# Kernel tuning notes

Hardware: AMD Instinct MI355X
Metric: run time of the kernel (lower is better)

The kernel has to match this reference:

```python
import jax, jax.numpy as jnp
import numpy as np

N_NODES = 40000
N_EDGES = 640000
IN_CH = 128
HID1, HID2 = 512, 256
OUT_CH = 2
NUM_GRAPHS = 16
EPS = 1e-5


def layer_norm(x, g, b):
    mu = jnp.mean(x, axis=-1, keepdims=True)
    var = jnp.mean(jnp.square(x - mu), axis=-1, keepdims=True)
    return (x - mu) * jax.lax.rsqrt(var + EPS) * g + b


def gcn_conv(x, src, dst, ew, W, b, n_nodes):
    # PyG GCNConv: x' = x @ W; symmetric normalization with self-loops already
    # appended to (src, dst, ew) by the caller; bias added after aggregation.
    xw = x @ W                                            # [N, out]
    deg = jax.ops.segment_sum(ew, dst, num_segments=n_nodes)
    dinv = jnp.where(deg > 0, jax.lax.rsqrt(deg), 0.0)    # deg^{-1/2}, 0 for isolated
    norm = dinv[src] * ew * dinv[dst]                     # [E+N]
    msgs = norm[:, None] * xw[src]                        # gather + scale
    out = jax.ops.segment_sum(msgs, dst, num_segments=n_nodes)
    return out + b


def setup_inputs() -> dict:
    key = jax.random.key(0)
    ks = jax.random.split(key, 12)
    x = jax.random.normal(ks[0], (N_NODES, IN_CH), dtype=jnp.float32)
    edge_index = jax.random.randint(ks[1], (2, N_EDGES), 0, N_NODES, dtype=jnp.int64)
    edge_weight = jax.random.uniform(ks[2], (N_EDGES,), dtype=jnp.float32)
    batch = jnp.sort(jax.random.randint(ks[3], (N_NODES,), 0, NUM_GRAPHS, dtype=jnp.int64))
    # parameters (Glorot-ish scale)
    W1 = jax.random.normal(ks[4], (IN_CH, HID1), dtype=jnp.float32) / np.sqrt(IN_CH)
    b1 = jnp.zeros((HID1,), dtype=jnp.float32)
    g1 = jnp.ones((HID1,), dtype=jnp.float32)
    be1 = jnp.zeros((HID1,), dtype=jnp.float32)
    W2 = jax.random.normal(ks[5], (HID1, HID2), dtype=jnp.float32) / np.sqrt(HID1)
    b2 = jnp.zeros((HID2,), dtype=jnp.float32)
    g2 = jnp.ones((HID2,), dtype=jnp.float32)
    be2 = jnp.zeros((HID2,), dtype=jnp.float32)
    Wfc = jax.random.normal(ks[6], (HID2, OUT_CH), dtype=jnp.float32) / np.sqrt(HID2)
    bfc = jnp.zeros((OUT_CH,), dtype=jnp.float32)
    return {"x": x, "edge_index": edge_index, "edge_weight": edge_weight,
            "batch": batch, "W1": W1, "b1": b1, "g1": g1, "be1": be1,
            "W2": W2, "b2": b2, "g2": g2, "be2": be2, "Wfc": Wfc, "bfc": bfc}


def reference(x, edge_index, edge_weight, batch, W1, b1, g1, be1, W2, b2, g2, be2, Wfc, bfc):
    n = x.shape[0]
    loop = jnp.arange(n, dtype=edge_index.dtype)
    src = jnp.concatenate([edge_index[0], loop])
    dst = jnp.concatenate([edge_index[1], loop])
    ew = jnp.concatenate([edge_weight, jnp.ones((n,), dtype=edge_weight.dtype)])

    h = gcn_conv(x, src, dst, ew, W1, b1, n)
    h = layer_norm(jax.nn.relu(h), g1, be1)          # dropout = identity (eval)
    h3 = gcn_conv(h, src, dst, ew, W2, b2, n)
    h3 = layer_norm(jax.nn.relu(h3), g2, be2)

    # global mean pool over graph ids
    sums = jax.ops.segment_sum(h3, batch, num_segments=NUM_GRAPHS)
    cnts = jax.ops.segment_sum(jnp.ones((n,), dtype=h3.dtype), batch, num_segments=NUM_GRAPHS)
    pooled = sums / jnp.maximum(cnts, 1.0)[:, None]
    out = pooled @ Wfc + bfc
    return h3, out
```

## Files before the change

kernel.cpp:

```cpp
#include <hip/hip_runtime.h>
#include <hip/hip_bf16.h>

#define N_NODES   40000
#define N_EDGES   640000
#define IN_CH     128
#define HID1      512
#define HID2      256
#define OUT_CH    2
#define NUM_GRAPHS 16
#define EPSF      1e-5f
#define SCAN_NB   157
#define FIXSC     1048576.0f

typedef unsigned short u16;
typedef unsigned int   u32;
typedef unsigned long long u64;
using short8 = __attribute__((ext_vector_type(8))) short;
using f32x4  = __attribute__((ext_vector_type(4))) float;

__device__ __forceinline__ float b2f(u16 u) {
    return __uint_as_float(((u32)u) << 16);
}
__device__ __forceinline__ u16 f2b(float f) {
    u32 u = __float_as_uint(f);
    u32 r = (u + 0x7FFFu + ((u >> 16) & 1u)) >> 16;
    return (u16)r;
}
__device__ __forceinline__ void gload_lds16(const u16* g, u16* l) {
    __builtin_amdgcn_global_load_lds((const __attribute__((address_space(1))) u32*)g,
                                     (__attribute__((address_space(3))) u32*)l, 16, 0, 0);
}

__global__ __launch_bounds__(256) void pack_kernel(const int* __restrict__ dst,
                                                   const float* __restrict__ ew,
                                                   u64* __restrict__ packed,
                                                   int* __restrict__ eoff) {
    int t = blockIdx.x * blockDim.x + threadIdx.x;
    if (t >= N_EDGES) return;
    int d = dst[t];
    u64 inc = (1ull << 40) | (u64)__float2uint_rn(ew[t] * FIXSC);
    u64 old = atomicAdd(&packed[d], inc);
    eoff[t] = (int)(old >> 40);
}

__global__ __launch_bounds__(256) void scan_p1_kernel(const u64* __restrict__ packed,
                                                      float* __restrict__ dinv,
                                                      int* __restrict__ rowptr,
                                                      int* __restrict__ blocksum) {
    __shared__ int sd[256];
    const int t = threadIdx.x;
    const int i = blockIdx.x * 256 + t;
    int v = 0;
    if (i < N_NODES) {
        u64 p = packed[i];
        v = (int)(p >> 40);
        float deg = (float)(p & ((1ull << 40) - 1)) * (1.0f / FIXSC);
        dinv[i] = rsqrtf(deg + 1.0f);
    }
    sd[t] = v;
    __syncthreads();
    for (int off = 1; off < 256; off <<= 1) {
        int u = (t >= off) ? sd[t - off] : 0;
        __syncthreads();
        sd[t] += u;
        __syncthreads();
    }
    if (i < N_NODES) rowptr[i] = sd[t] - v;
    if (t == 255) blocksum[blockIdx.x] = sd[255];
}

__global__ __launch_bounds__(256) void scan_p2_kernel(int* __restrict__ blocksum,
                                                      int* __restrict__ bprefix,
                                                      const int* __restrict__ batch,
                                                      int* __restrict__ gstart) {
    __shared__ int sd[256];
    const int t = threadIdx.x;
    const int v = (t < SCAN_NB) ? blocksum[t] : 0;
    sd[t] = v;
    __syncthreads();
    for (int off = 1; off < 256; off <<= 1) {
        int u = (t >= off) ? sd[t - off] : 0;
        __syncthreads();
        sd[t] += u;
        __syncthreads();
    }
    bprefix[t] = sd[t] - v;
    if (t <= NUM_GRAPHS) {
        int lo = 0, hi = N_NODES;
        while (lo < hi) {
            int mid = (lo + hi) >> 1;
            if (batch[mid] < t) lo = mid + 1; else hi = mid;
        }
        gstart[t] = lo;
    }
}

__global__ __launch_bounds__(256) void scan_p3_kernel(int* __restrict__ rowptr,
                                                      const int* __restrict__ bprefix) {
    const int i = blockIdx.x * 256 + threadIdx.x;
    if (i < N_NODES) rowptr[i] += bprefix[blockIdx.x];
    if (i == 0) rowptr[N_NODES] = N_EDGES;
}

__global__ __launch_bounds__(256) void scatter_kernel(const int* __restrict__ src,
                                                      const int* __restrict__ dst,
                                                      const float* __restrict__ ew,
                                                      const float* __restrict__ dinv,
                                                      const int* __restrict__ rowptr,
                                                      const int* __restrict__ eoff,
                                                      int2* __restrict__ csr_pair) {
    int t = blockIdx.x * blockDim.x + threadIdx.x;
    if (t >= N_EDGES) return;
    int s = src[t], d = dst[t];
    int pos = rowptr[d] + eoff[t];
    float norm = dinv[s] * ew[t] * dinv[d];
    int2 pr; pr.x = s; pr.y = __float_as_int(norm);
    csr_pair[pos] = pr;
}

__global__ __launch_bounds__(256) void prep_kernel(const float* __restrict__ x,
                                                   u16* __restrict__ xb,
                                                   const float* __restrict__ W1,
                                                   u16* __restrict__ W1T,
                                                   const float* __restrict__ W2,
                                                   u16* __restrict__ W2T) {
    int t = blockIdx.x * blockDim.x + threadIdx.x;
    if (t < N_NODES * IN_CH / 4) {
        float4 v = ((const float4*)x)[t];
        ushort4 o = { f2b(v.x), f2b(v.y), f2b(v.z), f2b(v.w) };
        ((ushort4*)xb)[t] = o;
    }
    if (t < IN_CH * HID1) {
        int r = t / HID1, c = t % HID1;
        W1T[(size_t)c * IN_CH + r] = f2b(W1[t]);
    }
    if (t < HID1 * HID2) {
        int r = t / HID2, c = t % HID2;
        W2T[(size_t)c * HID1 + r] = f2b(W2[t]);
    }
}

__global__ __launch_bounds__(256) void agg128_kernel(const int* __restrict__ rowptr,
                                                     const int2* __restrict__ csr_pair,
                                                     const float* __restrict__ dinv,
                                                     const u16* __restrict__ xb,
                                                     u16* __restrict__ outb) {
    const int node = (blockIdx.x * blockDim.x + threadIdx.x) >> 6;
    const int l = threadIdx.x & 63;
    if (node >= N_NODES) return;
    const int half = l >> 5, cl = l & 31;
    const float ds = dinv[node];
    const float wself = half ? 0.f : ds * ds;
    const int e0 = rowptr[node], e1 = rowptr[node + 1];
    const int c0 = cl * 4;

    ushort4 sv = *(const ushort4*)&xb[(size_t)node * IN_CH + c0];
    float acc[4] = { wself * b2f(sv.x), wself * b2f(sv.y),
                     wself * b2f(sv.z), wself * b2f(sv.w) };
    int e = e0;
    for (; e + 8 <= e1; e += 8) {
        int2 p[4]; ushort4 u[4];
#pragma unroll
        for (int j = 0; j < 4; ++j) p[j] = csr_pair[e + half + 2 * j];
#pragma unroll
        for (int j = 0; j < 4; ++j) u[j] = *(const ushort4*)&xb[(size_t)p[j].x * IN_CH + c0];
#pragma unroll
        for (int j = 0; j < 4; ++j) {
            float w = __int_as_float(p[j].y);
            acc[0] += w * b2f(u[j].x);
            acc[1] += w * b2f(u[j].y);
            acc[2] += w * b2f(u[j].z);
            acc[3] += w * b2f(u[j].w);
        }
    }
    for (int ee = e + half; ee < e1; ee += 2) {
        int2 p = csr_pair[ee];
        float w = __int_as_float(p.y);
        ushort4 u = *(const ushort4*)&xb[(size_t)p.x * IN_CH + c0];
        acc[0] += w * b2f(u.x);
        acc[1] += w * b2f(u.y);
        acc[2] += w * b2f(u.z);
        acc[3] += w * b2f(u.w);
    }
#pragma unroll
    for (int j = 0; j < 4; ++j) acc[j] += __shfl_xor(acc[j], 32);
    float a0 = half ? acc[2] : acc[0];
    float a1 = half ? acc[3] : acc[1];
    ushort2 o = { f2b(a0), f2b(a1) };
    *(ushort2*)&outb[(size_t)node * IN_CH + c0 + half * 2] = o;
}

__global__ __launch_bounds__(256) void agg256_ln_kernel(const int* __restrict__ rowptr,
                                                        const int2* __restrict__ csr_pair,
                                                        const float* __restrict__ dinv,
                                                        const u16* __restrict__ hwb,
                                                        const float* __restrict__ bias,
                                                        const float* __restrict__ g,
                                                        const float* __restrict__ be,
                                                        float* __restrict__ out) {
    const int node = (blockIdx.x * blockDim.x + threadIdx.x) >> 6;
    const int l = threadIdx.x & 63;
    if (node >= N_NODES) return;
    const int half = l >> 5, cl = l & 31;
    const float ds = dinv[node];
    const float wself = half ? 0.f : ds * ds;
    const int e0 = rowptr[node], e1 = rowptr[node + 1];
    const int c0 = cl * 8;

    short8 sv = *(const short8*)&hwb[(size_t)node * HID2 + c0];
    float acc[8];
#pragma unroll
    for (int j = 0; j < 8; ++j) acc[j] = wself * b2f((u16)sv[j]);

    int e = e0;
    for (; e + 8 <= e1; e += 8) {
        int2 p[4]; short8 u[4];
#pragma unroll
        for (int j = 0; j < 4; ++j) p[j] = csr_pair[e + half + 2 * j];
#pragma unroll
        for (int j = 0; j < 4; ++j) u[j] = *(const short8*)&hwb[(size_t)p[j].x * HID2 + c0];
#pragma unroll
        for (int j = 0; j < 4; ++j) {
            float w = __int_as_float(p[j].y);
#pragma unroll
            for (int k = 0; k < 8; ++k) acc[k] += w * b2f((u16)u[j][k]);
        }
    }
    for (int ee = e + half; ee < e1; ee += 2) {
        int2 p = csr_pair[ee];
        float w = __int_as_float(p.y);
        short8 u = *(const short8*)&hwb[(size_t)p.x * HID2 + c0];
#pragma unroll
        for (int k = 0; k < 8; ++k) acc[k] += w * b2f((u16)u[k]);
    }
#pragma unroll
    for (int j = 0; j < 8; ++j) acc[j] += __shfl_xor(acc[j], 32);

    float4 blo = *(const float4*)&bias[c0];
    float4 bhi = *(const float4*)&bias[c0 + 4];
    float vv[8];
    float sum = 0.f, sq = 0.f;
#pragma unroll
    for (int j = 0; j < 8; ++j) {
        float bj = (j < 4) ? ((const float*)&blo)[j] : ((const float*)&bhi)[j - 4];
        float xv = fmaxf(acc[j] + bj, 0.f);
        vv[j] = xv;
        sum += xv;
        sq += xv * xv;
    }
#pragma unroll
    for (int off = 1; off <= 16; off <<= 1) {
        sum += __shfl_xor(sum, off);
        sq  += __shfl_xor(sq, off);
    }
    const float mean = sum * (1.0f / HID2);
    const float var = sq * (1.0f / HID2) - mean * mean;
    const float r = rsqrtf(var + EPSF);

    const int cw = c0 + half * 4;
    float4 gq = *(const float4*)&g[cw];
    float4 bq = *(const float4*)&be[cw];
    float s0 = half ? vv[4] : vv[0];
    float s1 = half ? vv[5] : vv[1];
    float s2 = half ? vv[6] : vv[2];
    float s3 = half ? vv[7] : vv[3];
    float4 o;
    o.x = (s0 - mean) * r * gq.x + bq.x;
    o.y = (s1 - mean) * r * gq.y + bq.y;
    o.z = (s2 - mean) * r * gq.z + bq.z;
    o.w = (s3 - mean) * r * gq.w + bq.w;
    *(float4*)&out[(size_t)node * HID2 + cw] = o;
}

__global__ __launch_bounds__(512) void gemm1ln_kernel(const u16* __restrict__ A,
                                                      const u16* __restrict__ BT,
                                                      const float* __restrict__ b1,
                                                      const float* __restrict__ g1,
                                                      const float* __restrict__ be1,
                                                      u16* __restrict__ H) {
    __shared__ u16 As[64 * 32];
    __shared__ u16 Bs[512 * 32];
    __shared__ float lsum[8][64];
    __shared__ float lsq[8][64];
    __shared__ float lmean[64];
    __shared__ float lrstd[64];
    const int t = threadIdx.x;
    const int l = t & 63;
    const int wv = t >> 6;
    const int fr = l & 15;
    const int fg = l >> 4;
    const int rowbase = blockIdx.x * 64;

    f32x4 acc[4][4];
#pragma unroll
    for (int a = 0; a < 4; ++a)
#pragma unroll
        for (int b = 0; b < 4; ++b)
            acc[a][b] = (f32x4){0.f, 0.f, 0.f, 0.f};

    for (int k0 = 0; k0 < IN_CH; k0 += 32) {
        if (t < 256)
            gload_lds16(A + (size_t)(rowbase + (t >> 2)) * IN_CH + k0 + (t & 3) * 8,
                        As + t * 8);
#pragma unroll
        for (int j = 0; j < 4; ++j) {
            int c = t + 512 * j;
            gload_lds16(BT + (size_t)(c >> 2) * IN_CH + k0 + (c & 3) * 8,
                        Bs + c * 8);
        }
        __syncthreads();

        short8 af[4], bf[4];
#pragma unroll
        for (int fm = 0; fm < 4; ++fm)
            af[fm] = *(const short8*)&As[(fm * 16 + fr) * 32 + fg * 8];
#pragma unroll
        for (int fn = 0; fn < 4; ++fn)
            bf[fn] = *(const short8*)&Bs[(wv * 64 + fn * 16 + fr) * 32 + fg * 8];
#pragma unroll
        for (int fm = 0; fm < 4; ++fm)
#pragma unroll
            for (int fn = 0; fn < 4; ++fn)
                acc[fm][fn] = __builtin_amdgcn_mfma_f32_16x16x32_bf16(af[fm], bf[fn], acc[fm][fn], 0, 0, 0);
        __syncthreads();
    }

    const int colb = wv * 64;
    float bc[4], gc[4], bec[4];
#pragma unroll
    for (int fn = 0; fn < 4; ++fn) {
        int col = colb + fn * 16 + fr;
        bc[fn] = b1[col];
        gc[fn] = g1[col];
        bec[fn] = be1[col];
    }
    float ps[4][4], pq[4][4];
#pragma unroll
    for (int fm = 0; fm < 4; ++fm)
#pragma unroll
        for (int i = 0; i < 4; ++i) { ps[fm][i] = 0.f; pq[fm][i] = 0.f; }
#pragma unroll
    for (int fm = 0; fm < 4; ++fm)
#pragma unroll
        for (int fn = 0; fn < 4; ++fn)
#pragma unroll
            for (int i = 0; i < 4; ++i) {
                float xv = fmaxf(acc[fm][fn][i] + bc[fn], 0.f);
                acc[fm][fn][i] = xv;
                ps[fm][i] += xv;
                pq[fm][i] += xv * xv;
            }
#pragma unroll
    for (int off = 1; off < 16; off <<= 1)
#pragma unroll
        for (int fm = 0; fm < 4; ++fm)
#pragma unroll
            for (int i = 0; i < 4; ++i) {
                ps[fm][i] += __shfl_xor(ps[fm][i], off);
                pq[fm][i] += __shfl_xor(pq[fm][i], off);
            }
    if (fr == 0) {
#pragma unroll
        for (int fm = 0; fm < 4; ++fm)
#pragma unroll
            for (int i = 0; i < 4; ++i) {
                int row = fm * 16 + fg * 4 + i;
                lsum[wv][row] = ps[fm][i];
                lsq[wv][row] = pq[fm][i];
            }
    }
    __syncthreads();
    if (t < 64) {
        float s = 0.f, q = 0.f;
#pragma unroll
        for (int w = 0; w < 8; ++w) { s += lsum[w][t]; q += lsq[w][t]; }
        float mean = s * (1.0f / HID1);
        float var = q * (1.0f / HID1) - mean * mean;
        lmean[t] = mean;
        lrstd[t] = rsqrtf(var + EPSF);
    }
    __syncthreads();
#pragma unroll
    for (int fm = 0; fm < 4; ++fm)
#pragma unroll
        for (int fn = 0; fn < 4; ++fn)
#pragma unroll
            for (int i = 0; i < 4; ++i) {
                int row = fm * 16 + fg * 4 + i;
                int col = colb + fn * 16 + fr;
                float o = (acc[fm][fn][i] - lmean[row]) * lrstd[row] * gc[fn] + bec[fn];
                H[(size_t)(rowbase + row) * HID1 + col] = f2b(o);
            }
}

template <int K, int N, int ASTRIDE>
__global__ __launch_bounds__(256) void mfma_gemm128(const u16* __restrict__ A,
                                                    const u16* __restrict__ BT,
                                                    u16* __restrict__ Cb) {
    __shared__ u16 As[128 * 32];
    __shared__ u16 Bs[128 * 32];
    const int t = threadIdx.x;
    const int rowbase = blockIdx.x * 128;
    const int colbase = blockIdx.y * 128;
    const int l = t & 63;
    const int wv = t >> 6;
    const int wm = (wv >> 1) * 64;
    const int wn = (wv & 1) * 64;
    const int fr = l & 15;
    const int fg = l >> 4;

    f32x4 acc[4][4];
#pragma unroll
    for (int a = 0; a < 4; ++a)
#pragma unroll
        for (int b = 0; b < 4; ++b)
            acc[a][b] = (f32x4){0.f, 0.f, 0.f, 0.f};

    const int c0i = wv * 128 + l;
    const int c1i = c0i + 64;
    int ar0 = rowbase + (c0i >> 2); if (ar0 >= N_NODES) ar0 = N_NODES - 1;
    int ar1 = rowbase + (c1i >> 2); if (ar1 >= N_NODES) ar1 = N_NODES - 1;
    const u16* ag0 = A + (size_t)ar0 * ASTRIDE + (c0i & 3) * 8;
    const u16* ag1 = A + (size_t)ar1 * ASTRIDE + (c1i & 3) * 8;
    const u16* bg0 = BT + (size_t)(colbase + (c0i >> 2)) * K + (c0i & 3) * 8;
    const u16* bg1 = BT + (size_t)(colbase + (c1i >> 2)) * K + (c1i & 3) * 8;
    u16* al0 = As + c0i * 8;
    u16* al1 = As + c1i * 8;
    u16* bl0 = Bs + c0i * 8;
    u16* bl1 = Bs + c1i * 8;

    for (int k0 = 0; k0 < K; k0 += 32) {
        gload_lds16(ag0 + k0, al0);
        gload_lds16(ag1 + k0, al1);
        gload_lds16(bg0 + k0, bl0);
        gload_lds16(bg1 + k0, bl1);
        __syncthreads();

        short8 af[4], bf[4];
#pragma unroll
        for (int fm = 0; fm < 4; ++fm)
            af[fm] = *(const short8*)&As[(wm + fm * 16 + fr) * 32 + fg * 8];
#pragma unroll
        for (int fn = 0; fn < 4; ++fn)
            bf[fn] = *(const short8*)&Bs[(wn + fn * 16 + fr) * 32 + fg * 8];
#pragma unroll
        for (int fm = 0; fm < 4; ++fm)
#pragma unroll
            for (int fn = 0; fn < 4; ++fn)
                acc[fm][fn] = __builtin_amdgcn_mfma_f32_16x16x32_bf16(af[fm], bf[fn], acc[fm][fn], 0, 0, 0);
        __syncthreads();
    }

#pragma unroll
    for (int fm = 0; fm < 4; ++fm)
#pragma unroll
        for (int fn = 0; fn < 4; ++fn) {
#pragma unroll
            for (int i = 0; i < 4; ++i) {
                int row = rowbase + wm + fm * 16 + fg * 4 + i;
                if (row < N_NODES) {
                    int col = colbase + wn + fn * 16 + fr;
                    Cb[(size_t)row * N + col] = f2b(acc[fm][fn][i]);
                }
            }
        }
}

__global__ __launch_bounds__(256) void pool2_kernel(const float* __restrict__ h3,
                                                    const int* __restrict__ gstart,
                                                    float* __restrict__ part) {
    const int g = blockIdx.x, chunk = blockIdx.y;
    const int s = gstart[g], e = gstart[g + 1];
    const int len = e - s;
    const int c0 = s + (len * chunk) / 16;
    const int c1 = s + (len * (chunk + 1)) / 16;
    float acc = 0.f;
    for (int n = c0; n < c1; ++n)
        acc += h3[(size_t)n * HID2 + threadIdx.x];
    part[(size_t)(g * 16 + chunk) * HID2 + threadIdx.x] = acc;
}

__global__ __launch_bounds__(256) void fc_kernel(const float* __restrict__ part,
                                                 const int* __restrict__ gstart,
                                                 const float* __restrict__ Wfc,
                                                 const float* __restrict__ bfc,
                                                 float* __restrict__ out) {
    __shared__ float r0[256], r1[256];
    const int t = threadIdx.x;
    const float w0 = Wfc[t * 2], w1 = Wfc[t * 2 + 1];
    for (int g = 0; g < NUM_GRAPHS; ++g) {
        float v = 0.f;
#pragma unroll
        for (int k = 0; k < 16; ++k)
            v += part[(size_t)(g * 16 + k) * HID2 + t];
        r0[t] = v * w0;
        r1[t] = v * w1;
        __syncthreads();
        for (int off = 128; off >= 1; off >>= 1) {
            if (t < off) { r0[t] += r0[t + off]; r1[t] += r1[t + off]; }
            __syncthreads();
        }
        if (t == 0) {
            float inv = 1.0f / fmaxf((float)(gstart[g + 1] - gstart[g]), 1.0f);
            out[g * 2 + 0] = r0[0] * inv + bfc[0];
            out[g * 2 + 1] = r1[0] * inv + bfc[1];
        }
        __syncthreads();
    }
}

extern "C" void kernel_launch(void* const* d_in, const int* in_sizes, int n_in,
                              void* d_out, int out_size, void* d_ws, size_t ws_size,
                              hipStream_t stream) {
    const float* x   = (const float*)d_in[0];
    const int*   ei  = (const int*)d_in[1];
    const float* ew  = (const float*)d_in[2];
    const int*   bat = (const int*)d_in[3];
    const float* W1  = (const float*)d_in[4];
    const float* b1  = (const float*)d_in[5];
    const float* g1  = (const float*)d_in[6];
    const float* be1 = (const float*)d_in[7];
    const float* W2  = (const float*)d_in[8];
    const float* b2  = (const float*)d_in[9];
    const float* g2  = (const float*)d_in[10];
    const float* be2 = (const float*)d_in[11];
    const float* Wfc = (const float*)d_in[12];
    const float* bfc = (const float*)d_in[13];

    const int* srcArr = ei;
    const int* dstArr = ei + N_EDGES;

    float* out = (float*)d_out;
    float* h3  = out;
    float* fcO = out + (size_t)N_NODES * HID2;

    float* ws       = (float*)d_ws;
    u64*   packed   = (u64*)ws;
    float* dinv     = ws + 81920;
    int*   rowptr   = (int*)(ws + 122880);
    int*   gstart   = (int*)(ws + 163968);
    int*   blocksum = (int*)(ws + 164032);
    int*   bprefix  = (int*)(ws + 164288);
    int*   eoff     = (int*)(ws + 164544);
    int2*  csr_pair = (int2*)(ws + 804544);
    u16*   xb       = (u16*)(ws + 2084544);
    u16*   agg1b    = (u16*)(ws + 4644544);
    u16*   hb       = (u16*)(ws + 7204544);
    u16*   hwb      = (u16*)(ws + 17444544);
    u16*   W1T      = (u16*)(ws + 22564544);
    u16*   W2T      = (u16*)(ws + 22597312);
    float* part     = ws + 22662848;

    hipMemsetAsync(packed, 0, 40960 * sizeof(u64), stream);
    pack_kernel<<<(N_EDGES + 255) / 256, 256, 0, stream>>>(dstArr, ew, packed, eoff);
    scan_p1_kernel<<<SCAN_NB, 256, 0, stream>>>(packed, dinv, rowptr, blocksum);
    scan_p2_kernel<<<1, 256, 0, stream>>>(blocksum, bprefix, bat, gstart);
    scan_p3_kernel<<<SCAN_NB, 256, 0, stream>>>(rowptr, bprefix);
    scatter_kernel<<<(N_EDGES + 255) / 256, 256, 0, stream>>>(
        srcArr, dstArr, ew, dinv, rowptr, eoff, csr_pair);

    prep_kernel<<<(N_NODES * IN_CH / 4 + 255) / 256, 256, 0, stream>>>(
        x, xb, W1, W1T, W2, W2T);

    agg128_kernel<<<(N_NODES + 3) / 4, 256, 0, stream>>>(
        rowptr, csr_pair, dinv, xb, agg1b);
    gemm1ln_kernel<<<N_NODES / 64, 512, 0, stream>>>(agg1b, W1T, b1, g1, be1, hb);

    {
        dim3 grid((N_NODES + 127) / 128, HID2 / 128);
        mfma_gemm128<HID1, HID2, HID1><<<grid, 256, 0, stream>>>(hb, W2T, hwb);
    }
    agg256_ln_kernel<<<(N_NODES + 3) / 4, 256, 0, stream>>>(
        rowptr, csr_pair, dinv, hwb, b2, g2, be2, h3);

    {
        dim3 grid(NUM_GRAPHS, 16);
        pool2_kernel<<<grid, 256, 0, stream>>>(h3, gstart, part);
    }
    fc_kernel<<<1, 256, 0, stream>>>(part, gstart, Wfc, bfc, fcO);
}
```

Baseline: 261.5 us.

## Fuse edge packing with input conversion and widen gemm2 tile to full width

The edge-degree packing kernel and the bf16 conversion/transpose prep kernel are merged into one launch sized to the larger of the two index ranges. The second GEMM now uses 512-thread blocks that each compute a 128x256 output tile covering all output columns, so every A row tile is loaded once instead of twice. This removes one kernel launch and halves reads of the hidden activations in gemm2, at the cost of larger blocks and more LDS per block, which may lower occupancy.

```diff
diff --git a/kernel.cpp b/kernel.cpp
--- a/kernel.cpp
+++ b/kernel.cpp
@@ -31,16 +31,36 @@
                                      (__attribute__((address_space(3))) u32*)l, 16, 0, 0);
 }
 
-__global__ __launch_bounds__(256) void pack_kernel(const int* __restrict__ dst,
-                                                   const float* __restrict__ ew,
-                                                   u64* __restrict__ packed,
-                                                   int* __restrict__ eoff) {
+__global__ __launch_bounds__(256) void packprep_kernel(const int* __restrict__ dst,
+                                                       const float* __restrict__ ew,
+                                                       u64* __restrict__ packed,
+                                                       int* __restrict__ eoff,
+                                                       const float* __restrict__ x,
+                                                       u16* __restrict__ xb,
+                                                       const float* __restrict__ W1,
+                                                       u16* __restrict__ W1T,
+                                                       const float* __restrict__ W2,
+                                                       u16* __restrict__ W2T) {
     int t = blockIdx.x * blockDim.x + threadIdx.x;
-    if (t >= N_EDGES) return;
-    int d = dst[t];
-    u64 inc = (1ull << 40) | (u64)__float2uint_rn(ew[t] * FIXSC);
-    u64 old = atomicAdd(&packed[d], inc);
-    eoff[t] = (int)(old >> 40);
+    if (t < N_EDGES) {
+        int d = dst[t];
+        u64 inc = (1ull << 40) | (u64)__float2uint_rn(ew[t] * FIXSC);
+        u64 old = atomicAdd(&packed[d], inc);
+        eoff[t] = (int)(old >> 40);
+    }
+    if (t < N_NODES * IN_CH / 4) {
+        float4 v = ((const float4*)x)[t];
+        ushort4 o = { f2b(v.x), f2b(v.y), f2b(v.z), f2b(v.w) };
+        ((ushort4*)xb)[t] = o;
+    }
+    if (t < IN_CH * HID1) {
+        int r = t / HID1, c = t % HID1;
+        W1T[(size_t)c * IN_CH + r] = f2b(W1[t]);
+    }
+    if (t < HID1 * HID2) {
+        int r = t / HID2, c = t % HID2;
+        W2T[(size_t)c * HID1 + r] = f2b(W2[t]);
+    }
 }
 
 __global__ __launch_bounds__(256) void scan_p1_kernel(const u64* __restrict__ packed,
@@ -116,28 +136,6 @@
     float norm = dinv[s] * ew[t] * dinv[d];
     int2 pr; pr.x = s; pr.y = __float_as_int(norm);
     csr_pair[pos] = pr;
-}
-
-__global__ __launch_bounds__(256) void prep_kernel(const float* __restrict__ x,
-                                                   u16* __restrict__ xb,
-                                                   const float* __restrict__ W1,
-                                                   u16* __restrict__ W1T,
-                                                   const float* __restrict__ W2,
-                                                   u16* __restrict__ W2T) {
-    int t = blockIdx.x * blockDim.x + threadIdx.x;
-    if (t < N_NODES * IN_CH / 4) {
-        float4 v = ((const float4*)x)[t];
-        ushort4 o = { f2b(v.x), f2b(v.y), f2b(v.z), f2b(v.w) };
-        ((ushort4*)xb)[t] = o;
-    }
-    if (t < IN_CH * HID1) {
-        int r = t / HID1, c = t % HID1;
-        W1T[(size_t)c * IN_CH + r] = f2b(W1[t]);
-    }
-    if (t < HID1 * HID2) {
-        int r = t / HID2, c = t % HID2;
-        W2T[(size_t)c * HID1 + r] = f2b(W2[t]);
-    }
 }
 
 __global__ __launch_bounds__(256) void agg128_kernel(const int* __restrict__ rowptr,
@@ -393,21 +391,19 @@
             }
 }
 
-template <int K, int N, int ASTRIDE>
-__global__ __launch_bounds__(256) void mfma_gemm128(const u16* __restrict__ A,
+__global__ __launch_bounds__(512) void gemm2_kernel(const u16* __restrict__ A,
                                                     const u16* __restrict__ BT,
                                                     u16* __restrict__ Cb) {
     __shared__ u16 As[128 * 32];
-    __shared__ u16 Bs[128 * 32];
+    __shared__ u16 Bs[256 * 32];
     const int t = threadIdx.x;
-    const int rowbase = blockIdx.x * 128;
-    const int colbase = blockIdx.y * 128;
     const int l = t & 63;
     const int wv = t >> 6;
-    const int wm = (wv >> 1) * 64;
-    const int wn = (wv & 1) * 64;
+    const int wm = (wv >> 2) * 64;
+    const int wn = (wv & 3) * 64;
     const int fr = l & 15;
     const int fg = l >> 4;
+    const int rowbase = blockIdx.x * 128;
 
     f32x4 acc[4][4];
 #pragma unroll
@@ -416,24 +412,16 @@
         for (int b = 0; b < 4; ++b)
             acc[a][b] = (f32x4){0.f, 0.f, 0.f, 0.f};
 
-    const int c0i = wv * 128 + l;
-    const int c1i = c0i + 64;
-    int ar0 = rowbase + (c0i >> 2); if (ar0 >= N_NODES) ar0 = N_NODES - 1;
-    int ar1 = rowbase + (c1i >> 2); if (ar1 >= N_NODES) ar1 = N_NODES - 1;
-    const u16* ag0 = A + (size_t)ar0 * ASTRIDE + (c0i & 3) * 8;
-    const u16* ag1 = A + (size_t)ar1 * ASTRIDE + (c1i & 3) * 8;
-    const u16* bg0 = BT + (size_t)(colbase + (c0i >> 2)) * K + (c0i & 3) * 8;
-    const u16* bg1 = BT + (size_t)(colbase + (c1i >> 2)) * K + (c1i & 3) * 8;
-    u16* al0 = As + c0i * 8;
-    u16* al1 = As + c1i * 8;
-    u16* bl0 = Bs + c0i * 8;
-    u16* bl1 = Bs + c1i * 8;
-
-    for (int k0 = 0; k0 < K; k0 += 32) {
-        gload_lds16(ag0 + k0, al0);
-        gload_lds16(ag1 + k0, al1);
-        gload_lds16(bg0 + k0, bl0);
-        gload_lds16(bg1 + k0, bl1);
+    int ar = rowbase + (t >> 2); if (ar >= N_NODES) ar = N_NODES - 1;
+    const u16* ag = A + (size_t)ar * HID1 + (t & 3) * 8;
+    const int cb0 = t, cb1 = t + 512;
+    const u16* bg0 = BT + (size_t)(cb0 >> 2) * HID1 + (cb0 & 3) * 8;
+    const u16* bg1 = BT + (size_t)(cb1 >> 2) * HID1 + (cb1 & 3) * 8;
+
+    for (int k0 = 0; k0 < HID1; k0 += 32) {
+        gload_lds16(ag + k0, As + t * 8);
+        gload_lds16(bg0 + k0, Bs + cb0 * 8);
+        gload_lds16(bg1 + k0, Bs + cb1 * 8);
         __syncthreads();
 
         short8 af[4], bf[4];
@@ -459,8 +447,8 @@
             for (int i = 0; i < 4; ++i) {
                 int row = rowbase + wm + fm * 16 + fg * 4 + i;
                 if (row < N_NODES) {
-                    int col = colbase + wn + fn * 16 + fr;
-                    Cb[(size_t)row * N + col] = f2b(acc[fm][fn][i]);
+                    int col = wn + fn * 16 + fr;
+                    Cb[(size_t)row * HID2 + col] = f2b(acc[fm][fn][i]);
                 }
             }
         }
@@ -552,24 +540,20 @@
     float* part     = ws + 22662848;
 
     hipMemsetAsync(packed, 0, 40960 * sizeof(u64), stream);
-    pack_kernel<<<(N_EDGES + 255) / 256, 256, 0, stream>>>(dstArr, ew, packed, eoff);
+    packprep_kernel<<<(N_NODES * IN_CH / 4 + 255) / 256, 256, 0, stream>>>(
+        dstArr, ew, packed, eoff, x, xb, W1, W1T, W2, W2T);
+
     scan_p1_kernel<<<SCAN_NB, 256, 0, stream>>>(packed, dinv, rowptr, blocksum);
     scan_p2_kernel<<<1, 256, 0, stream>>>(blocksum, bprefix, bat, gstart);
     scan_p3_kernel<<<SCAN_NB, 256, 0, stream>>>(rowptr, bprefix);
     scatter_kernel<<<(N_EDGES + 255) / 256, 256, 0, stream>>>(
         srcArr, dstArr, ew, dinv, rowptr, eoff, csr_pair);
 
-    prep_kernel<<<(N_NODES * IN_CH / 4 + 255) / 256, 256, 0, stream>>>(
-        x, xb, W1, W1T, W2, W2T);
-
     agg128_kernel<<<(N_NODES + 3) / 4, 256, 0, stream>>>(
         rowptr, csr_pair, dinv, xb, agg1b);
     gemm1ln_kernel<<<N_NODES / 64, 512, 0, stream>>>(agg1b, W1T, b1, g1, be1, hb);
 
-    {
-        dim3 grid((N_NODES + 127) / 128, HID2 / 128);
-        mfma_gemm128<HID1, HID2, HID1><<<grid, 256, 0, stream>>>(hb, W2T, hwb);
-    }
+    gemm2_kernel<<<(N_NODES + 127) / 128, 512, 0, stream>>>(hb, W2T, hwb);
     agg256_ln_kernel<<<(N_NODES + 3) / 4, 256, 0, stream>>>(
         rowptr, csr_pair, dinv, hwb, b2, g2, be2, h3);
 
```

Measured after the change: 258.8 us (median of 2 runs). Within noise of the previous version (-1.1%).
